# Kernel tuning notes

Hardware: AMD Instinct MI355X
Metric: run time of the kernel (lower is better)

## Reference

```python
import math
import jax, jax.numpy as jnp
import numpy as np

H = 16          # num attention heads
D = 64          # head dim
BUCKETS = 256   # position_buckets
MAX_POS = 512   # max_relative_positions
ATT_SPAN = BUCKETS  # pos_ebd_size A
SCALE_FACTOR = 3    # 1 + len(['c2p','p2c'])


def _log_bucket(rel):
    # log-bucketed relative positions (DeBERTa-v2 _make_log_bucket_position)
    mid = BUCKETS // 2
    rel = jnp.clip(rel, -MAX_POS + 1, MAX_POS - 1)
    sign = jnp.sign(rel).astype(jnp.float32)
    abs_pos = jnp.maximum(jnp.abs(rel), 1)
    log_base = math.log((MAX_POS - 1) / mid)
    log_pos = jnp.ceil(jnp.log(abs_pos.astype(jnp.float32) / mid) / log_base * (mid - 1)) + mid
    bucket = jnp.where(abs_pos < mid, abs_pos.astype(jnp.float32), log_pos) * sign
    return bucket.astype(jnp.int32)


def _rel_pos(q_len, k_len):
    q = jnp.arange(q_len, dtype=jnp.int32)
    k = jnp.arange(k_len, dtype=jnp.int32)
    return _log_bucket(q[:, None] - k[None, :])  # (Q, K)


def setup_inputs() -> dict:
    key = jax.random.key(0)
    ks = jax.random.split(key, 6)
    B, S, Hd = 4, 1024, 1024
    std = 0.02
    return {
        "hidden_states": jax.random.normal(ks[0], (B, S, Hd), jnp.float32),
        "rel_embeddings": jax.random.normal(ks[1], (2 * ATT_SPAN, Hd), jnp.float32) * std,
        "Wq": jax.random.normal(ks[2], (Hd, H * D), jnp.float32) * std,
        "bq": jnp.zeros((H * D,), jnp.float32),
        "Wk": jax.random.normal(ks[3], (Hd, H * D), jnp.float32) * std,
        "bk": jnp.zeros((H * D,), jnp.float32),
        "Wv": jax.random.normal(ks[4], (Hd, H * D), jnp.float32) * std,
        "bv": jnp.zeros((H * D,), jnp.float32),
    }


def reference(hidden_states, rel_embeddings, Wq, bq, Wk, bk, Wv, bv):
    B, S, Hd = hidden_states.shape
    A2 = 2 * ATT_SPAN

    def heads(x):  # (B,S,H*D) -> (B,H,S,D)
        return x.reshape(B, S, H, D).transpose(0, 2, 1, 3)

    q = heads(hidden_states @ Wq + bq)
    k = heads(hidden_states @ Wk + bk)
    v = heads(hidden_states @ Wv + bv)

    scale = math.sqrt(D * SCALE_FACTOR)
    scores = jnp.einsum('bhqd,bhkd->bhqk', q, k) / scale  # (B,H,S,S)

    rel = _rel_pos(S, S)  # (S,S) int32 bucketed relative ids
    # share_att_key=True: pos key/query use key_proj/query_proj
    pos_k = (rel_embeddings @ Wk + bk).reshape(A2, H, D).transpose(1, 0, 2)  # (H,2A,D)
    pos_q = (rel_embeddings @ Wq + bq).reshape(A2, H, D).transpose(1, 0, 2)  # (H,2A,D)

    # c2p: content->position
    c2p = jnp.einsum('bhqd,hkd->bhqk', q, pos_k)  # (B,H,S,2A)
    c2p_idx = jnp.clip(rel + ATT_SPAN, 0, A2 - 1)  # (S,S)
    c2p = jnp.take_along_axis(c2p, jnp.broadcast_to(c2p_idx[None, None], (B, H, S, S)), axis=-1) / scale

    # p2c: position->content
    p2c = jnp.einsum('bhkd,hqd->bhkq', k, pos_q)  # (B,H,S,2A)
    p2c_idx = jnp.clip(-rel + ATT_SPAN, 0, A2 - 1)  # (S,S)
    p2c = jnp.take_along_axis(p2c, jnp.broadcast_to(p2c_idx[None, None], (B, H, S, S)), axis=-1)
    p2c = jnp.swapaxes(p2c, -1, -2) / scale

    probs = jax.nn.softmax(scores + c2p + p2c, axis=-1)
    ctx = jnp.einsum('bhqk,bhkd->bhqd', probs, v)  # (B,H,S,D)
    return ctx.transpose(0, 2, 1, 3).reshape(B, S, H * D)
```

## Files before the change

### kernel.cpp

```cpp
#include <hip/hip_runtime.h>
#include <hip/hip_bf16.h>
#include <math.h>

typedef __attribute__((ext_vector_type(8))) short v8s;
typedef __attribute__((ext_vector_type(4))) short v4sh;
typedef __attribute__((ext_vector_type(4))) unsigned short v4us;
typedef __attribute__((ext_vector_type(4))) float v4f;
typedef __attribute__((ext_vector_type(4))) int   v4i;

#define AS1(p) ((const __attribute__((address_space(1))) void*)(p))
#define AS3(p) ((__attribute__((address_space(3))) void*)(p))

__device__ inline unsigned short f2b(float f){
  __hip_bfloat16 h = __float2bfloat16(f);
  return __builtin_bit_cast(unsigned short, h);
}
__device__ inline float b2f(unsigned short u){
  __hip_bfloat16 h = __builtin_bit_cast(__hip_bfloat16, u);
  return __bfloat162float(h);
}
__device__ inline unsigned cvtpk(float lo, float hi){
  unsigned d;
  asm("v_cvt_pk_bf16_f32 %0, %1, %2" : "=v"(d) : "v"(lo), "v"(hi));
  return d;
}

__device__ inline int bucket_id(int i){
  int r = i - 1023;
  if (r > 511) r = 511; if (r < -511) r = -511;
  float sign = (r > 0) ? 1.f : ((r < 0) ? -1.f : 0.f);
  int ap = r < 0 ? -r : r; if (ap < 1) ap = 1;
  float bucket;
  if (ap < 128) bucket = (float)ap * sign;
  else {
    float lp = ceilf(logf((float)ap / 128.f) / logf(511.f/128.f) * 127.f) + 128.f;
    bucket = lp * sign;
  }
  int idx = (int)bucket + 256;
  if (idx < 0) idx = 0; if (idx > 511) idx = 511;
  return idx;
}

__global__ __launch_bounds__(256) void pack_x(const float* __restrict__ hs,
                                              const float* __restrict__ rel,
                                              const float* __restrict__ Wq,
                                              const float* __restrict__ Wk,
                                              const float* __restrict__ Wv,
                                              unsigned short* __restrict__ X,
                                              unsigned short* __restrict__ Wt3,
                                              short* __restrict__ tab,
                                              unsigned long long* __restrict__ tab64){
  __shared__ unsigned short t[64][65];
  int blk = blockIdx.x;
  if (blk < 2304){
    const int HT8 = 4096*1024/8;
    int i8 = blk*256 + threadIdx.x;
    const float* src = (i8 < HT8) ? (hs + (size_t)i8*8) : (rel + ((size_t)i8 - HT8)*8);
    v8s o;
    #pragma unroll
    for (int j = 0; j < 8; j++) o[j] = (short)f2b(src[j]);
    *(v8s*)&X[(size_t)i8*8] = o;
    return;
  }
  if (blk < 2313){
    int i = (blk - 2304)*256 + threadIdx.x;
    if (i < 2047) tab[i] = (short)bucket_id(i);
    if (i < 2056){
      unsigned long long w = 0;
      #pragma unroll
      for (int r = 0; r < 4; r++)
        w |= (unsigned long long)(unsigned short)bucket_id(i + r) << (16*r);
      tab64[i] = w;
    }
    return;
  }
  int tb = blk - 2313;
  int wsel = tb >> 8, bx = tb & 255;
  const float* in = (wsel == 0) ? Wq : ((wsel == 1) ? Wk : Wv);
  unsigned short* outp = Wt3 + ((size_t)wsel << 20);
  int r0 = (bx >> 4) << 6, c0 = (bx & 15) << 6;
  int tx = threadIdx.x & 63, ty = threadIdx.x >> 6;
  #pragma unroll
  for (int p = 0; p < 16; p++){ int r = (p<<2)+ty; t[tx][r] = f2b(in[(size_t)(r0+r)*1024 + c0+tx]); }
  __syncthreads();
  #pragma unroll
  for (int p = 0; p < 16; p++){ int c = (p<<2)+ty; outp[(size_t)(c0+c)*1024 + r0+tx] = t[c][tx]; }
}

__global__ __launch_bounds__(256) void gemm_qkv(
    const unsigned short* __restrict__ A,
    const unsigned short* __restrict__ Bt3,
    unsigned short* __restrict__ Qa, unsigned short* __restrict__ Ka,
    unsigned short* __restrict__ VtT,
    const float* __restrict__ bq, const float* __restrict__ bk,
    const float* __restrict__ bv, float alpha_q)
{
  __shared__ unsigned short smem[2*128*64];
  unsigned short* a_tile = smem;
  unsigned short* b_tile = smem + 128*64;
  int nb = (blockIdx.x & 7)*108 + (blockIdx.x >> 3);
  int bm = nb / 24, bn = nb % 24;
  int m0 = bm << 7, n0 = bn << 7;
  int tid = threadIdx.x, lane = tid & 63, wave = tid >> 6;
  int l15 = lane & 15, lhi = lane >> 4;
  int rbase = (wave >> 1) << 6, cbase = (wave & 1) << 6;
  int crow[4], csw[4];
  #pragma unroll
  for (int u = 0; u < 4; u++){
    int ch = tid + (u << 8);
    crow[u] = ch >> 3;
    csw[u] = ((ch & 7) ^ (crow[u] & 7)) << 3;
  }
  v4f acc[4][4] = {};
  for (int kt = 0; kt < 1024; kt += 64){
    #pragma unroll
    for (int u = 0; u < 4; u++){
      int ch = tid + (u << 8);
      __builtin_amdgcn_global_load_lds(AS1(A   + (size_t)(m0 + crow[u])*1024 + kt + csw[u]),
                                       AS3(a_tile + (size_t)ch*8), 16, 0, 0);
      __builtin_amdgcn_global_load_lds(AS1(Bt3 + (size_t)(n0 + crow[u])*1024 + kt + csw[u]),
                                       AS3(b_tile + (size_t)ch*8), 16, 0, 0);
    }
    __syncthreads();
    #pragma unroll
    for (int ks = 0; ks < 2; ks++){
      v8s af[4], bfr[4];
      int kb = (ks << 2) + lhi;
      #pragma unroll
      for (int i = 0; i < 4; i++){
        int r = rbase + (i << 4) + l15;
        af[i] = *(const v8s*)&a_tile[r*64 + ((kb ^ (r & 7)) << 3)];
      }
      #pragma unroll
      for (int j = 0; j < 4; j++){
        int r = cbase + (j << 4) + l15;
        bfr[j] = *(const v8s*)&b_tile[r*64 + ((kb ^ (r & 7)) << 3)];
      }
      #pragma unroll
      for (int i = 0; i < 4; i++)
        #pragma unroll
        for (int j = 0; j < 4; j++)
          acc[i][j] = __builtin_amdgcn_mfma_f32_16x16x32_bf16(af[i], bfr[j], acc[i][j], 0, 0, 0);
    }
    __syncthreads();
  }
  int seg = n0 >> 10;
  int nn0 = n0 & 1023;
  if (seg == 2){
    if (m0 >= 4096) return;
    int bb = m0 >> 10, s0 = m0 & 1023;
    #pragma unroll
    for (int i = 0; i < 4; i++){
      int r = rbase + (i << 4) + (lhi << 2);
      #pragma unroll
      for (int j = 0; j < 4; j++){
        int c = cbase + (j << 4) + l15;
        float bvv = bv[nn0 + c];
        #pragma unroll
        for (int rr = 0; rr < 4; rr++)
          smem[c*128 + ((r + rr) ^ ((c & 7) << 4))] = f2b(acc[i][j][rr] + bvv);
      }
    }
    __syncthreads();
    int v = tid >> 3, sc = (tid & 7) << 4;
    #pragma unroll
    for (int vb = 0; vb < 4; vb++){
      int vv = v + (vb << 5);
      #pragma unroll
      for (int c2 = 0; c2 < 2; c2++){
        int sb = sc + (c2 << 3);
        v8s val = *(const v8s*)&smem[vv*128 + (sb ^ ((vv & 7) << 4))];
        *(v8s*)&VtT[((size_t)(bb << 10) + nn0 + vv)*1024 + s0 + sb] = val;
      }
    }
    return;
  }
  unsigned short* C = (seg == 0) ? Qa : Ka;
  const float* bias = (seg == 0) ? bq : bk;
  float alpha = (seg == 0) ? alpha_q : 1.f;
  #pragma unroll
  for (int i = 0; i < 4; i++){
    int row = rbase + (i << 4) + (lhi << 2);
    #pragma unroll
    for (int j = 0; j < 4; j++){
      int col = cbase + (j << 4) + l15;
      float bvv = bias[nn0 + col];
      #pragma unroll
      for (int r = 0; r < 4; r++)
        smem[(row + r)*128 + (col ^ (((row + r) & 7) << 4))] = f2b((acc[i][j][r] + bvv) * alpha);
    }
  }
  __syncthreads();
  #pragma unroll
  for (int c = 0; c < 8; c++){
    int row = (tid >> 4) + (c << 4);
    int col8 = (tid & 15) << 3;
    v8s val = *(const v8s*)&smem[row*128 + (col8 ^ ((row & 7) << 4))];
    *(v8s*)&C[(size_t)(m0 + row)*1024 + nn0 + col8] = val;
  }
}

__global__ __launch_bounds__(256) void gemm_pos(
    const unsigned short* __restrict__ Qa,
    const unsigned short* __restrict__ Ka,
    unsigned short* __restrict__ C2P,
    unsigned short* __restrict__ P2C)
{
  __shared__ unsigned short smem[2*128*64];
  unsigned short* a_tile = smem;
  unsigned short* b_tile = smem + 128*64;
  int tab = blockIdx.y >> 4, h = blockIdx.y & 15;
  int bm = blockIdx.x >> 2, bn = blockIdx.x & 3;
  int m0 = bm << 7, n0 = bn << 7;
  const unsigned short* A  = tab ? Ka : Qa;
  const unsigned short* Bt = tab ? Qa : Ka;
  unsigned short* C = tab ? P2C : C2P;
  int tid = threadIdx.x, lane = tid & 63, wave = tid >> 6;
  int l15 = lane & 15, lhi = lane >> 4;
  int rbase = (wave >> 1) << 6, cbase = (wave & 1) << 6;
  #pragma unroll
  for (int u = 0; u < 4; u++){
    int ch = tid + (u << 8);
    int row = ch >> 3;
    int csw = ((ch & 7) ^ (row & 7)) << 3;
    __builtin_amdgcn_global_load_lds(AS1(A  + (size_t)(m0 + row)*1024 + (h << 6) + csw),
                                     AS3(a_tile + (size_t)ch*8), 16, 0, 0);
    __builtin_amdgcn_global_load_lds(AS1(Bt + (size_t)(4096 + n0 + row)*1024 + (h << 6) + csw),
                                     AS3(b_tile + (size_t)ch*8), 16, 0, 0);
  }
  __syncthreads();
  v4f acc[4][4] = {};
  #pragma unroll
  for (int ks = 0; ks < 2; ks++){
    v8s af[4], bfr[4];
    int kb = (ks << 2) + lhi;
    #pragma unroll
    for (int i = 0; i < 4; i++){
      int r = rbase + (i << 4) + l15;
      af[i] = *(const v8s*)&a_tile[r*64 + ((kb ^ (r & 7)) << 3)];
    }
    #pragma unroll
    for (int j = 0; j < 4; j++){
      int r = cbase + (j << 4) + l15;
      bfr[j] = *(const v8s*)&b_tile[r*64 + ((kb ^ (r & 7)) << 3)];
    }
    #pragma unroll
    for (int i = 0; i < 4; i++)
      #pragma unroll
      for (int j = 0; j < 4; j++)
        acc[i][j] = __builtin_amdgcn_mfma_f32_16x16x32_bf16(af[i], bfr[j], acc[i][j], 0, 0, 0);
  }
  __syncthreads();
  #pragma unroll
  for (int i = 0; i < 4; i++){
    int row = rbase + (i << 4) + (lhi << 2);
    #pragma unroll
    for (int j = 0; j < 4; j++){
      int col = cbase + (j << 4) + l15;
      #pragma unroll
      for (int r = 0; r < 4; r++)
        smem[(row + r)*128 + (col ^ (((row + r) & 7) << 4))] = f2b(acc[i][j][r]);
    }
  }
  __syncthreads();
  #pragma unroll
  for (int c = 0; c < 8; c++){
    int row = (tid >> 4) + (c << 4);
    int col8 = (tid & 15) << 3;
    v8s val = *(const v8s*)&smem[row*128 + (col8 ^ ((row & 7) << 4))];
    *(v8s*)&C[(size_t)(m0 + row)*8192 + (h << 9) + n0 + col8] = val;
  }
}

__global__ __launch_bounds__(256) void attn(
  const unsigned short* __restrict__ Qall,
  const unsigned short* __restrict__ Kall,
  const unsigned short* __restrict__ Vt,
  const unsigned short* __restrict__ c2p,
  const unsigned short* __restrict__ p2c,
  const short* __restrict__ idxt,
  const unsigned long long* __restrict__ t64g,
  float* __restrict__ out)
{
  __shared__ unsigned short k_lds[64*64];
  __shared__ unsigned short v_lds[64*64];
  __shared__ unsigned short cw[128*72];
  __shared__ unsigned short pw[64*144];
  __shared__ short basc[16*128];
  __shared__ short basp[16*64];

  int bid = blockIdx.x;
  int xcd = bid & 7, jj = bid >> 3;
  int bh = (xcd << 3) + (jj >> 3), qb = jj & 7;
  int b = bh >> 4, h = bh & 15;
  int q0 = qb << 7;
  int tid = threadIdx.x, lane = tid & 63, wave = tid >> 6;
  int l15 = lane & 15, lhi = lane >> 4;

  #pragma unroll
  for (int v = 0; v < 12; v++){
    int i = tid + (v << 8);
    if (i < 2048){
      int kt = i >> 7, row = i & 127;
      int bc = idxt[q0 + row - (kt << 6) + 960] & ~7;
      basc[i] = (short)(row*72 - bc);
    } else {
      int i2 = i - 2048;
      int kt = i2 >> 6, row = i2 & 63;
      int bp = idxt[q0 + 1023 - (kt << 6) - row] & ~7;
      basp[i2] = (short)(row*144 - bp);
    }
  }

  v8s aq[2][2];
  #pragma unroll
  for (int g = 0; g < 2; g++)
    #pragma unroll
    for (int ks = 0; ks < 2; ks++)
      aq[g][ks] = *(const v8s*)&Qall[(size_t)((b << 10) + q0 + (wave << 5) + (g << 4) + l15)*1024
                                     + (h << 6) + (ks << 5) + (lhi << 3)];

  const size_t cbase0 = ((size_t)((b << 10) + q0))*8192 + (h << 9);
  const size_t pbase0 = ((size_t)(b << 10))*8192 + (h << 9);

  unsigned long long t64u[2][4];

  auto issue_kwin = [&](int kt){
    int k0 = kt << 6;
    #pragma unroll
    for (int u = 0; u < 2; u++){
      int ch = tid + (u << 8);
      int rr = ch >> 3, seg = ch & 7;
      int csw = (seg ^ (rr & 7)) << 3;
      __builtin_amdgcn_global_load_lds(AS1(Kall + (size_t)((b << 10) + k0 + rr)*1024 + (h << 6) + csw),
                                       AS3(k_lds + (size_t)ch*8), 16, 0, 0);
    }
    #pragma unroll
    for (int u = 0; u < 5; u++){
      int pp = tid + (u << 8);
      if (pp < 1152){
        int row = pp / 9, cc = pp - row*9;
        int bc = row*72 - (int)basc[(kt << 7) + row];
        __builtin_amdgcn_global_load_lds(AS1(c2p + cbase0 + (size_t)row*8192 + bc + (cc << 3)),
                                         AS3(cw + (size_t)pp*8), 16, 0, 0);
      }
    }
    #pragma unroll
    for (int u = 0; u < 5; u++){
      int pp = tid + (u << 8);
      if (pp < 1152){
        int row = pp / 18, cc = pp - row*18;
        int bp = row*144 - (int)basp[(kt << 6) + row];
        __builtin_amdgcn_global_load_lds(AS1(p2c + pbase0 + (size_t)(k0 + row)*8192 + bp + (cc << 3)),
                                         AS3(pw + (size_t)pp*8), 16, 0, 0);
      }
    }
  };
  auto issue_tv = [&](int kt){
    int k0 = kt << 6;
    #pragma unroll
    for (int g = 0; g < 2; g++){
      int Bc = q0 - k0 + (wave << 5) + (g << 4) + l15 - (lhi << 2) + 1020;
      #pragma unroll
      for (int j = 0; j < 4; j++) t64u[g][j] = t64g[Bc - (j << 4)];
    }
    __builtin_amdgcn_sched_barrier(0);
    #pragma unroll
    for (int u = 0; u < 2; u++){
      int ch = tid + (u << 8);
      int rr = ch >> 3, seg = ch & 7;
      int csw = (seg ^ (rr & 7)) << 3;
      __builtin_amdgcn_global_load_lds(AS1(Vt + (size_t)((b << 10) + (h << 6) + rr)*1024 + k0 + csw),
                                       AS3(v_lds + (size_t)ch*8), 16, 0, 0);
    }
  };

  v4f o_acc[4][2] = {};
  float m_run[2] = { -INFINITY, -INFINITY };
  float l_part[2] = { 0.f, 0.f };

  __syncthreads();
  issue_kwin(0);
  __builtin_amdgcn_sched_barrier(0);
  issue_tv(0);

  for (int kt = 0; kt < 16; kt++){
    asm volatile("s_waitcnt vmcnt(10)" ::: "memory");
    __builtin_amdgcn_sched_barrier(0);
    __builtin_amdgcn_s_barrier();
    __builtin_amdgcn_sched_barrier(0);

    v4f s_acc[4][2] = {};
    __builtin_amdgcn_s_setprio(1);
    #pragma unroll
    for (int j = 0; j < 4; j++){
      int krow = (j << 4) + l15;
      #pragma unroll
      for (int ks = 0; ks < 2; ks++){
        v8s kf = *(const v8s*)&k_lds[krow*64 + ((((ks << 2) + lhi) ^ (krow & 7)) << 3)];
        s_acc[j][0] = __builtin_amdgcn_mfma_f32_16x16x32_bf16(kf, aq[0][ks], s_acc[j][0], 0, 0, 0);
        s_acc[j][1] = __builtin_amdgcn_mfma_f32_16x16x32_bf16(kf, aq[1][ks], s_acc[j][1], 0, 0, 0);
      }
    }
    __builtin_amdgcn_s_setprio(0);
    int cvq0 = (int)basc[(kt << 7) + (wave << 5) + l15];
    int cvq1 = (int)basc[(kt << 7) + (wave << 5) + 16 + l15];
    #pragma unroll
    for (int j = 0; j < 4; j++){
      v4sh bp4 = *(const v4sh*)&basp[(kt << 6) + (j << 4) + (lhi << 2)];
      v4us id0 = __builtin_bit_cast(v4us, t64u[0][j]);
      v4us id1 = __builtin_bit_cast(v4us, t64u[1][j]);
      #pragma unroll
      for (int r = 0; r < 4; r++){
        int pwb = (int)bp4[r];
        int ida = (int)id0[3 - r];
        int idb = (int)id1[3 - r];
        s_acc[j][0][r] += b2f(cw[cvq0 + ida]) + b2f(pw[pwb + ida]);
        s_acc[j][1][r] += b2f(cw[cvq1 + idb]) + b2f(pw[pwb + idb]);
      }
    }
    float lmax[2];
    #pragma unroll
    for (int g = 0; g < 2; g++){
      float lm = s_acc[0][g][0];
      #pragma unroll
      for (int j = 0; j < 4; j++)
        #pragma unroll
        for (int r = 0; r < 4; r++) lm = fmaxf(lm, s_acc[j][g][r]);
      lmax[g] = lm;
    }
    if (__any((lmax[0] > m_run[0] + 6.f) || (lmax[1] > m_run[1] + 6.f))){
      #pragma unroll
      for (int g = 0; g < 2; g++){
        float mx = lmax[g];
        mx = fmaxf(mx, __shfl_xor(mx, 16));
        mx = fmaxf(mx, __shfl_xor(mx, 32));
        float mnew = fmaxf(m_run[g], mx);
        float corr = exp2f(m_run[g] - mnew);
        m_run[g] = mnew;
        l_part[g] *= corr;
        float co[4];
        #pragma unroll
        for (int r = 0; r < 4; r++) co[r] = __shfl(corr, (lhi << 2) + r);
        #pragma unroll
        for (int j = 0; j < 4; j++)
          #pragma unroll
          for (int r = 0; r < 4; r++) o_acc[j][g][r] *= co[r];
      }
    }
    v8s pa0[2], pa1[2];
    #pragma unroll
    for (int g = 0; g < 2; g++){
      unsigned wj[4][2];
      float ps = 0.f;
      #pragma unroll
      for (int j = 0; j < 4; j++){
        float p0 = exp2f(s_acc[j][g][0] - m_run[g]);
        float p1 = exp2f(s_acc[j][g][1] - m_run[g]);
        float p2 = exp2f(s_acc[j][g][2] - m_run[g]);
        float p3 = exp2f(s_acc[j][g][3] - m_run[g]);
        ps += (p0 + p1) + (p2 + p3);
        wj[j][0] = cvtpk(p0, p1);
        wj[j][1] = cvtpk(p2, p3);
      }
      l_part[g] += ps;
      #pragma unroll
      for (int p = 0; p < 2; p++){
        asm("v_permlane32_swap_b32 %0, %1" : "+v"(wj[0][p]), "+v"(wj[1][p]));
        asm("v_permlane32_swap_b32 %0, %1" : "+v"(wj[2][p]), "+v"(wj[3][p]));
        asm("v_permlane16_swap_b32 %0, %1" : "+v"(wj[0][p]), "+v"(wj[1][p]));
        asm("v_permlane16_swap_b32 %0, %1" : "+v"(wj[2][p]), "+v"(wj[3][p]));
      }
      v4i pai0 = { (int)wj[0][0], (int)wj[0][1], (int)wj[1][0], (int)wj[1][1] };
      v4i pai1 = { (int)wj[2][0], (int)wj[2][1], (int)wj[3][0], (int)wj[3][1] };
      pa0[g] = __builtin_bit_cast(v8s, pai0);
      pa1[g] = __builtin_bit_cast(v8s, pai1);
    }

    asm volatile("s_waitcnt vmcnt(0)" ::: "memory");
    __builtin_amdgcn_sched_barrier(0);
    __builtin_amdgcn_s_barrier();
    __builtin_amdgcn_sched_barrier(0);

    if (kt < 15) issue_kwin(kt + 1);
    __builtin_amdgcn_sched_barrier(0);

    __builtin_amdgcn_s_setprio(1);
    #pragma unroll
    for (int j = 0; j < 4; j++){
      int vrow = (j << 4) + l15;
      v8s vb0 = *(const v8s*)&v_lds[vrow*64 + (((lhi) ^ (vrow & 7)) << 3)];
      v8s vb1 = *(const v8s*)&v_lds[vrow*64 + (((4 + lhi) ^ (vrow & 7)) << 3)];
      o_acc[j][0] = __builtin_amdgcn_mfma_f32_16x16x32_bf16(pa0[0], vb0, o_acc[j][0], 0, 0, 0);
      o_acc[j][1] = __builtin_amdgcn_mfma_f32_16x16x32_bf16(pa0[1], vb0, o_acc[j][1], 0, 0, 0);
      o_acc[j][0] = __builtin_amdgcn_mfma_f32_16x16x32_bf16(pa1[0], vb1, o_acc[j][0], 0, 0, 0);
      o_acc[j][1] = __builtin_amdgcn_mfma_f32_16x16x32_bf16(pa1[1], vb1, o_acc[j][1], 0, 0, 0);
    }
    __builtin_amdgcn_s_setprio(0);
    if (kt < 15){
      asm volatile("s_waitcnt lgkmcnt(0)" ::: "memory");
      __builtin_amdgcn_sched_barrier(0);
      __builtin_amdgcn_s_barrier();
      __builtin_amdgcn_sched_barrier(0);
      issue_tv(kt + 1);
    }
  }
  #pragma unroll
  for (int g = 0; g < 2; g++){
    float ls = l_part[g];
    ls += __shfl_xor(ls, 16);
    ls += __shfl_xor(ls, 32);
    float inv = 1.f / ls;
    float io[4];
    #pragma unroll
    for (int r = 0; r < 4; r++) io[r] = __shfl(inv, (lhi << 2) + r);
    #pragma unroll
    for (int r = 0; r < 4; r++){
      int row = q0 + (wave << 5) + (g << 4) + (lhi << 2) + r;
      #pragma unroll
      for (int j = 0; j < 4; j++)
        out[(size_t)((b << 10) + row)*1024 + (h << 6) + (j << 4) + l15] = o_acc[j][g][r] * io[r];
    }
  }
}

extern "C" void kernel_launch(void* const* d_in, const int* in_sizes, int n_in,
                              void* d_out, int out_size, void* d_ws, size_t ws_size,
                              hipStream_t stream)
{
  const float* hs  = (const float*)d_in[0];
  const float* rel = (const float*)d_in[1];
  const float* Wq  = (const float*)d_in[2];
  const float* bq  = (const float*)d_in[3];
  const float* Wk  = (const float*)d_in[4];
  const float* bk  = (const float*)d_in[5];
  const float* Wv  = (const float*)d_in[6];
  const float* bv  = (const float*)d_in[7];
  float* out = (float*)d_out;

  char* ws = (char*)d_ws;
  size_t off = 0;
  auto alloc = [&](size_t bytes) -> void* {
    void* p = ws + off; off += (bytes + 255) & ~(size_t)255; return p;
  };
  short*              idxt  = (short*)             alloc(2047 * 2);
  unsigned long long* tab64 = (unsigned long long*)alloc(2056 * 8);
  unsigned short* Xb   = (unsigned short*)alloc((size_t)4608*1024*2);
  unsigned short* Wt3  = (unsigned short*)alloc((size_t)3072*1024*2);
  unsigned short* Qa   = (unsigned short*)alloc((size_t)4608*1024*2);
  unsigned short* Ka   = (unsigned short*)alloc((size_t)4608*1024*2);
  unsigned short* VtT  = (unsigned short*)alloc((size_t)4096*1024*2);
  unsigned short* C2P  = (unsigned short*)alloc((size_t)4096*8192*2);
  unsigned short* P2C  = (unsigned short*)alloc((size_t)4096*8192*2);
  (void)                                  alloc(4096);
  (void)ws_size; (void)in_sizes; (void)n_in; (void)out_size;

  pack_x<<<3081, 256, 0, stream>>>(hs, rel, Wq, Wk, Wv, Xb, Wt3, idxt, tab64);

  const float alpha_q = 1.4426950408889634f / sqrtf(192.f);
  gemm_qkv<<<864, 256, 0, stream>>>(Xb, Wt3, Qa, Ka, VtT, bq, bk, bv, alpha_q);

  gemm_pos<<<dim3(128, 32), 256, 0, stream>>>(Qa, Ka, C2P, P2C);

  attn<<<512, 256, 0, stream>>>(Qa, Ka, VtT, C2P, P2C, idxt, tab64, out);
}
```

Baseline: 155.4 us.

## Load V fragments directly into registers and pad p2c LDS rows

V tiles are now loaded from global memory straight into per-wave registers instead of being staged through shared memory. This removes the V LDS buffer and one block barrier per iteration. The p2c window's LDS row stride grows from 144 to 152 elements, which likely reduces bank conflicts. Wait counts are adjusted to match. The risk is that the register loads now sit in the critical path right before the PV MFMAs, register pressure rises, and the vmcnt bookkeeping may not wait on the right loads.

```diff
diff --git a/kernel.cpp b/kernel.cpp
--- a/kernel.cpp
+++ b/kernel.cpp
@@ -283,9 +283,8 @@
   float* __restrict__ out)
 {
   __shared__ unsigned short k_lds[64*64];
-  __shared__ unsigned short v_lds[64*64];
   __shared__ unsigned short cw[128*72];
-  __shared__ unsigned short pw[64*144];
+  __shared__ unsigned short pw[64*152];
   __shared__ short basc[16*128];
   __shared__ short basp[16*64];
 
@@ -308,7 +307,7 @@
       int i2 = i - 2048;
       int kt = i2 >> 6, row = i2 & 63;
       int bp = idxt[q0 + 1023 - (kt << 6) - row] & ~7;
-      basp[i2] = (short)(row*144 - bp);
+      basp[i2] = (short)(row*152 - bp);
     }
   }
 
@@ -322,8 +321,10 @@
 
   const size_t cbase0 = ((size_t)((b << 10) + q0))*8192 + (h << 9);
   const size_t pbase0 = ((size_t)(b << 10))*8192 + (h << 9);
+  const size_t vrow0  = ((size_t)(b << 10) + (h << 6) + l15)*1024 + (lhi << 3);
 
   unsigned long long t64u[2][4];
+  v8s vr0[4], vr1[4];
 
   auto issue_kwin = [&](int kt){
     int k0 = kt << 6;
@@ -350,9 +351,9 @@
       int pp = tid + (u << 8);
       if (pp < 1152){
         int row = pp / 18, cc = pp - row*18;
-        int bp = row*144 - (int)basp[(kt << 6) + row];
+        int bp = row*152 - (int)basp[(kt << 6) + row];
         __builtin_amdgcn_global_load_lds(AS1(p2c + pbase0 + (size_t)(k0 + row)*8192 + bp + (cc << 3)),
-                                         AS3(pw + (size_t)pp*8), 16, 0, 0);
+                                         AS3(pw + (size_t)(row*152 + (cc << 3))*1), 16, 0, 0);
       }
     }
   };
@@ -366,12 +367,9 @@
     }
     __builtin_amdgcn_sched_barrier(0);
     #pragma unroll
-    for (int u = 0; u < 2; u++){
-      int ch = tid + (u << 8);
-      int rr = ch >> 3, seg = ch & 7;
-      int csw = (seg ^ (rr & 7)) << 3;
-      __builtin_amdgcn_global_load_lds(AS1(Vt + (size_t)((b << 10) + (h << 6) + rr)*1024 + k0 + csw),
-                                       AS3(v_lds + (size_t)ch*8), 16, 0, 0);
+    for (int j = 0; j < 4; j++){
+      vr0[j] = *(const v8s*)&Vt[vrow0 + (size_t)(j << 4)*1024 + k0];
+      vr1[j] = *(const v8s*)&Vt[vrow0 + (size_t)(j << 4)*1024 + k0 + 32];
     }
   };
 
@@ -385,7 +383,7 @@
   issue_tv(0);
 
   for (int kt = 0; kt < 16; kt++){
-    asm volatile("s_waitcnt vmcnt(10)" ::: "memory");
+    asm volatile("s_waitcnt vmcnt(16)" ::: "memory");
     __builtin_amdgcn_sched_barrier(0);
     __builtin_amdgcn_s_barrier();
     __builtin_amdgcn_sched_barrier(0);
@@ -477,7 +475,7 @@
       pa1[g] = __builtin_bit_cast(v8s, pai1);
     }
 
-    asm volatile("s_waitcnt vmcnt(0)" ::: "memory");
+    asm volatile("s_waitcnt lgkmcnt(0)" ::: "memory");
     __builtin_amdgcn_sched_barrier(0);
     __builtin_amdgcn_s_barrier();
     __builtin_amdgcn_sched_barrier(0);
@@ -488,22 +486,14 @@
     __builtin_amdgcn_s_setprio(1);
     #pragma unroll
     for (int j = 0; j < 4; j++){
-      int vrow = (j << 4) + l15;
-      v8s vb0 = *(const v8s*)&v_lds[vrow*64 + (((lhi) ^ (vrow & 7)) << 3)];
-      v8s vb1 = *(const v8s*)&v_lds[vrow*64 + (((4 + lhi) ^ (vrow & 7)) << 3)];
-      o_acc[j][0] = __builtin_amdgcn_mfma_f32_16x16x32_bf16(pa0[0], vb0, o_acc[j][0], 0, 0, 0);
-      o_acc[j][1] = __builtin_amdgcn_mfma_f32_16x16x32_bf16(pa0[1], vb0, o_acc[j][1], 0, 0, 0);
-      o_acc[j][0] = __builtin_amdgcn_mfma_f32_16x16x32_bf16(pa1[0], vb1, o_acc[j][0], 0, 0, 0);
-      o_acc[j][1] = __builtin_amdgcn_mfma_f32_16x16x32_bf16(pa1[1], vb1, o_acc[j][1], 0, 0, 0);
+      o_acc[j][0] = __builtin_amdgcn_mfma_f32_16x16x32_bf16(pa0[0], vr0[j], o_acc[j][0], 0, 0, 0);
+      o_acc[j][1] = __builtin_amdgcn_mfma_f32_16x16x32_bf16(pa0[1], vr0[j], o_acc[j][1], 0, 0, 0);
+      o_acc[j][0] = __builtin_amdgcn_mfma_f32_16x16x32_bf16(pa1[0], vr1[j], o_acc[j][0], 0, 0, 0);
+      o_acc[j][1] = __builtin_amdgcn_mfma_f32_16x16x32_bf16(pa1[1], vr1[j], o_acc[j][1], 0, 0, 0);
     }
     __builtin_amdgcn_s_setprio(0);
-    if (kt < 15){
-      asm volatile("s_waitcnt lgkmcnt(0)" ::: "memory");
-      __builtin_amdgcn_sched_barrier(0);
-      __builtin_amdgcn_s_barrier();
-      __builtin_amdgcn_sched_barrier(0);
-      issue_tv(kt + 1);
-    }
+    __builtin_amdgcn_sched_barrier(0);
+    if (kt < 15) issue_tv(kt + 1);
   }
   #pragma unroll
   for (int g = 0; g < 2; g++){
```

After: 209.3 us. +34.7%, slower.
